# Kernel optimization log

Measured on AMD Instinct MI355X. Metric: run time of the kernel, lower is better.

The kernel has to match this reference:

```python
import jax, jax.numpy as jnp
import numpy as np

S, B, N, F, E, H, GH = 32, 64, 2048, 16, 32768, 512, 1
RNN_FEAT = N * GH
EPS = 1e-5


def setup_inputs() -> dict:
    key = jax.random.key(0)
    ks = jax.random.split(key, 24)
    f = lambda i, shape, s=0.1: (jax.random.normal(ks[i], shape, dtype=jnp.float32) * s)
    inp = {
        "x": jax.random.normal(ks[0], (S, B, N, F), dtype=jnp.float32),
        "edge_index": jax.random.randint(ks[1], (2, E), 0, N, dtype=jnp.int64),
        # GCNConv layers
        "W1": f(2, (F, GH)), "b1": f(3, (GH,)),
        "W2": f(4, (GH, GH)), "b2": f(5, (GH,)),
        # BatchNorm1d (eval mode: running stats)
        "gamma": jnp.ones((RNN_FEAT,), jnp.float32),
        "beta": jnp.zeros((RNN_FEAT,), jnp.float32),
        "rmean": f(6, (RNN_FEAT,), 0.01),
        "rvar": jnp.ones((RNN_FEAT,), jnp.float32),
        # GRU layer 0 (input RNN_FEAT -> hidden H)
        "Wih0": f(7, (3 * H, RNN_FEAT), 0.02), "Whh0": f(8, (3 * H, H), 0.02),
        "bih0": f(9, (3 * H,), 0.02), "bhh0": f(10, (3 * H,), 0.02),
        # GRU layer 1 (H -> H)
        "Wih1": f(11, (3 * H, H), 0.02), "Whh1": f(12, (3 * H, H), 0.02),
        "bih1": f(13, (3 * H,), 0.02), "bhh1": f(14, (3 * H,), 0.02),
        # final Linear(H -> 1)
        "Wlin": f(15, (1, H), 0.05), "blin": f(16, (1,), 0.05),
    }
    return inp


def _gru_layer(inp, Wih, Whh, bih, bhh):
    Hh = Whh.shape[1]

    def step(hprev, xt):
        gi = xt @ Wih.T + bih          # (B, 3H)
        gh = hprev @ Whh.T + bhh       # (B, 3H)
        ir, iz, inn = jnp.split(gi, 3, axis=-1)
        hr, hz, hn = jnp.split(gh, 3, axis=-1)
        r = jax.nn.sigmoid(ir + hr)
        z = jax.nn.sigmoid(iz + hz)
        n = jnp.tanh(inn + r * hn)
        hnew = (1.0 - z) * n + z * hprev
        return hnew, hnew

    h0 = jnp.zeros((inp.shape[1], Hh), dtype=inp.dtype)
    hT, ys = jax.lax.scan(step, h0, inp)
    return ys, hT


def reference(x, edge_index, W1, b1, W2, b2, gamma, beta, rmean, rvar,
              Wih0, Whh0, bih0, bhh0, Wih1, Whh1, bih1, bhh1, Wlin, blin):
    Sx, Bx, Nx, Fx = x.shape
    loop = jnp.arange(Nx, dtype=edge_index.dtype)
    src = jnp.concatenate([edge_index[0], loop])  # self-loops (GCNConv default)
    dst = jnp.concatenate([edge_index[1], loop])
    deg = jax.ops.segment_sum(jnp.ones_like(src, dtype=x.dtype), dst, num_segments=Nx)
    dinv = jax.lax.rsqrt(deg)  # deg >= 1 thanks to self-loops
    norm = dinv[src] * dinv[dst]  # (E+N,)

    def conv(h, W, b):
        h = h @ W                                           # (SB, N, F')
        m = (h[:, src, :] * norm[None, :, None])            # (SB, E+N, F')
        agg = jax.ops.segment_sum(m.transpose(1, 0, 2), dst, num_segments=Nx)
        return agg.transpose(1, 0, 2) + b                   # (SB, N, F')

    xr = x.reshape(Sx * Bx, Nx, Fx)
    h = jax.nn.sigmoid(conv(xr, W1, b1))   # dropout is identity in eval mode
    h = conv(h, W2, b2)                    # (SB, N, GH)
    o = h.reshape(Sx, Bx, Nx * h.shape[-1])
    # BatchNorm1d, eval mode
    o = (o - rmean) * jax.lax.rsqrt(rvar + EPS) * gamma + beta

    y1, h1 = _gru_layer(o, Wih0, Whh0, bih0, bhh0)
    y2, h2 = _gru_layer(y1, Wih1, Whh1, bih1, bhh1)
    out = y2 @ Wlin.T + blin               # (S, B, 1)
    hn = jnp.stack([h1, h2])               # (n_layers, B, H)
    return out, hn
```

## Files before the change

kernel.cpp:

```cpp
#include <hip/hip_runtime.h>
#include <stdint.h>

#define S_DIM 32
#define B_DIM 64
#define N_DIM 2048
#define F_DIM 16
#define E_DIM 32768
#define H_DIM 512
#define H3 1536
#define SB 2048
#define EPS_BN 1e-5f
#define GRUB 256

typedef __attribute__((ext_vector_type(4))) float f32x4;
typedef __attribute__((ext_vector_type(8))) __bf16 bf16x8;

static __device__ __forceinline__ unsigned short f2bf(float f) {
    union { float f; unsigned int u; } v; v.f = f;
    unsigned int r = v.u + 0x7FFFu + ((v.u >> 16) & 1u);
    return (unsigned short)(r >> 16);
}

#define HLD(dst, base, OFF) \
    asm volatile("global_load_dword %0, %1, off offset:" #OFF " sc0 sc1" : "=v"(dst) : "v"(base))
#define HLD16(A, I, base) \
    HLD(A[I+0],base,0);    HLD(A[I+1],base,256);  HLD(A[I+2],base,512);  HLD(A[I+3],base,768); \
    HLD(A[I+4],base,1024); HLD(A[I+5],base,1280); HLD(A[I+6],base,1536); HLD(A[I+7],base,1792); \
    HLD(A[I+8],base,2048); HLD(A[I+9],base,2304); HLD(A[I+10],base,2560);HLD(A[I+11],base,2816);\
    HLD(A[I+12],base,3072);HLD(A[I+13],base,3328);HLD(A[I+14],base,3584);HLD(A[I+15],base,3840)
#define HST(val, addr) \
    asm volatile("global_store_dword %0, %1, off sc0 sc1" :: "v"(addr), "v"(val) : "memory")

__global__ __launch_bounds__(256) void k_gcn1_dot(const float* __restrict__ x,
        const float* __restrict__ W1, float* __restrict__ z) {
    __shared__ float tile[64][65];
    int bn = blockIdx.x & 31;
    int bs = blockIdx.x >> 5;
    int n0 = bn * 64, sb0 = bs * 64;
    float4 w0 = *(const float4*)&W1[0];
    float4 w1 = *(const float4*)&W1[4];
    float4 w2 = *(const float4*)&W1[8];
    float4 w3 = *(const float4*)&W1[12];
    int t = threadIdx.x;
    for (int i = 0; i < 16; ++i) {
        int idx = t + 256 * i;
        int nl = idx & 63, sl = idx >> 6;
        const float4* xv = (const float4*)(x + ((size_t)(sb0 + sl) * N_DIM + (n0 + nl)) * F_DIM);
        float4 a = xv[0], b = xv[1], c = xv[2], d = xv[3];
        float acc = a.x*w0.x + a.y*w0.y + a.z*w0.z + a.w*w0.w
                  + b.x*w1.x + b.y*w1.y + b.z*w1.z + b.w*w1.w
                  + c.x*w2.x + c.y*w2.y + c.z*w2.z + c.w*w2.w
                  + d.x*w3.x + d.y*w3.y + d.z*w3.z + d.w*w3.w;
        tile[nl][sl] = acc;
    }
    __syncthreads();
    for (int i = 0; i < 16; ++i) {
        int idx = t + 256 * i;
        int sl = idx & 63, nl = idx >> 6;
        z[(size_t)(n0 + nl) * SB + sb0 + sl] = tile[nl][sl];
    }
}

__global__ void k_degcnt(const int* __restrict__ ei, int* __restrict__ cnt) {
    int e = blockIdx.x * 256 + threadIdx.x;
    if (e < E_DIM) atomicAdd(&cnt[ei[E_DIM + e]], 1);
}
__global__ void k_dinv(const int* __restrict__ cnt, float* __restrict__ dinv) {
    int n = blockIdx.x * 256 + threadIdx.x;
    if (n < N_DIM) dinv[n] = rsqrtf(1.0f + (float)cnt[n]);
}
__global__ void k_scan(const int* __restrict__ cnt, int* __restrict__ rowptr) {
    __shared__ int sc[2048];
    int t = threadIdx.x;
    sc[t] = cnt[t]; sc[t + 1024] = cnt[t + 1024];
    __syncthreads();
    for (int off = 1; off < 2048; off <<= 1) {
        int a = (t >= off) ? sc[t - off] : 0;
        int b = (t + 1024 >= off) ? sc[t + 1024 - off] : 0;
        __syncthreads();
        sc[t] += a; sc[t + 1024] += b;
        __syncthreads();
    }
    rowptr[t] = sc[t] - cnt[t];
    rowptr[t + 1024] = sc[t + 1024] - cnt[t + 1024];
    if (t == 0) rowptr[2048] = E_DIM;
}
__global__ void k_fill(const int* __restrict__ ei, const int* __restrict__ rowptr,
                       int* __restrict__ cursor, int* __restrict__ cols) {
    int e = blockIdx.x * 256 + threadIdx.x;
    if (e < E_DIM) {
        int d = ei[E_DIM + e];
        int pos = atomicAdd(&cursor[d], 1);
        cols[rowptr[d] + pos] = ei[e];
    }
}

__global__ __launch_bounds__(256) void k_spmm(const float* __restrict__ in,
        float* __restrict__ outp, const int* __restrict__ rowptr, const int* __restrict__ cols,
        const float* __restrict__ dinv, int mode,
        const float* __restrict__ bp, const float* __restrict__ w2p,
        const float* __restrict__ gamma, const float* __restrict__ beta,
        const float* __restrict__ rmean, const float* __restrict__ rvar) {
    int n = blockIdx.x & 2047;
    int sb = ((blockIdx.x >> 11) << 8) + threadIdx.x;
    float dn = dinv[n];
    float acc = dn * dn * in[(size_t)n * SB + sb];
    int i0 = rowptr[n], i1 = rowptr[n + 1];
    for (int idx = i0; idx < i1; ++idx) {
        int s = cols[idx];
        acc += dn * dinv[s] * in[(size_t)s * SB + sb];
    }
    float v;
    if (mode == 0) {
        v = acc + bp[0];
        v = 1.0f / (1.0f + __expf(-v));
    } else {
        v = w2p[0] * acc + bp[0];
        v = (v - rmean[n]) * rsqrtf(rvar[n] + EPS_BN) * gamma[n] + beta[n];
    }
    outp[(size_t)n * SB + sb] = v;
}

__global__ __launch_bounds__(256) void k_transpose_cvt(const float* __restrict__ in,
        unsigned short* __restrict__ outp, int R, int C) {
    __shared__ float tile[64][65];
    int nrt = R >> 6;
    int rt = blockIdx.x % nrt;
    int ct = blockIdx.x / nrt;
    int r0 = rt * 64, c0 = ct * 64;
    int t = threadIdx.x;
    for (int i = 0; i < 16; ++i) {
        int idx = t + i * 256;
        int cl = idx & 63, rl = idx >> 6;
        tile[rl][cl] = in[(size_t)(r0 + rl) * C + c0 + cl];
    }
    __syncthreads();
    for (int i = 0; i < 16; ++i) {
        int idx = t + i * 256;
        int rl = idx & 63, cl = idx >> 6;
        outp[(size_t)(c0 + cl) * R + r0 + rl] = f2bf(tile[rl][cl]);
    }
}

__global__ __launch_bounds__(256) void k_transpose_f32(const float* __restrict__ in,
        float* __restrict__ outp, int R, int C) {
    __shared__ float tile[64][65];
    int nrt = R >> 6;
    int rt = blockIdx.x % nrt;
    int ct = blockIdx.x / nrt;
    int r0 = rt * 64, c0 = ct * 64;
    int t = threadIdx.x;
    for (int i = 0; i < 16; ++i) {
        int idx = t + i * 256;
        int cl = idx & 63, rl = idx >> 6;
        tile[rl][cl] = in[(size_t)(r0 + rl) * C + c0 + cl];
    }
    __syncthreads();
    for (int i = 0; i < 16; ++i) {
        int idx = t + i * 256;
        int rl = idx & 63, cl = idx >> 6;
        outp[(size_t)(c0 + cl) * R + r0 + rl] = tile[rl][cl];
    }
}

__global__ void k_cvt_bf16(const float* __restrict__ in, unsigned short* __restrict__ outp, int nelem) {
    int i = (blockIdx.x * 256 + threadIdx.x) * 4;
    if (i < nelem) {
        float4 v = *(const float4*)&in[i];
        ushort4 o;
        o.x = f2bf(v.x); o.y = f2bf(v.y); o.z = f2bf(v.z); o.w = f2bf(v.w);
        *(ushort4*)&outp[i] = o;
    }
}

#define BM 128
#define BN 64
#define BKK 32
#define LDT 40

__global__ __launch_bounds__(256) void k_gemm_bf16(
        const unsigned short* __restrict__ A,
        const unsigned short* __restrict__ Bm,
        const float* __restrict__ bias,
        float* __restrict__ Cm, int M, int N, int K) {
    __shared__ __align__(16) unsigned short lA[BM * LDT];
    __shared__ __align__(16) unsigned short lB[BN * LDT];
    int mtiles = M / BM;
    int mt = blockIdx.x % mtiles;
    int nt = blockIdx.x / mtiles;
    int m0 = mt * BM, n0 = nt * BN;
    int t = threadIdx.x;
    int wave = t >> 6, lane = t & 63;
    int wm = (wave >> 1) * 64, wn = (wave & 1) * 32;
    int lrow = lane & 15, lk = (lane >> 4) * 8;
    int srowA = t >> 1, scolA = (t & 1) * 16;
    int srowB = t >> 2, scolB = (t & 3) * 8;
    f32x4 acc[4][2] = {};
    for (int k0 = 0; k0 < K; k0 += BKK) {
        const unsigned short* ga = A  + (size_t)(m0 + srowA) * K + k0 + scolA;
        const unsigned short* gb = Bm + (size_t)(n0 + srowB) * K + k0 + scolB;
        *(uint4*)&lA[srowA * LDT + scolA]     = *(const uint4*)ga;
        *(uint4*)&lA[srowA * LDT + scolA + 8] = *(const uint4*)(ga + 8);
        *(uint4*)&lB[srowB * LDT + scolB]     = *(const uint4*)gb;
        __syncthreads();
        bf16x8 af[4], bg[2];
        #pragma unroll
        for (int i = 0; i < 4; ++i)
            af[i] = *(const bf16x8*)&lA[(wm + i * 16 + lrow) * LDT + lk];
        #pragma unroll
        for (int j = 0; j < 2; ++j)
            bg[j] = *(const bf16x8*)&lB[(wn + j * 16 + lrow) * LDT + lk];
        #pragma unroll
        for (int i = 0; i < 4; ++i)
            #pragma unroll
            for (int j = 0; j < 2; ++j)
                acc[i][j] = __builtin_amdgcn_mfma_f32_16x16x32_bf16(af[i], bg[j], acc[i][j], 0, 0, 0);
        __syncthreads();
    }
    int crow = (lane >> 4) * 4, ccol = lane & 15;
    #pragma unroll
    for (int i = 0; i < 4; ++i)
        #pragma unroll
        for (int j = 0; j < 2; ++j) {
            int gn = n0 + wn + j * 16 + ccol;
            float bv = bias[gn];
            #pragma unroll
            for (int r = 0; r < 4; ++r) {
                int gm = m0 + wm + i * 16 + crow + r;
                Cm[(size_t)gm * N + gn] = acc[i][j][r] + bv;
            }
        }
}

__global__ __launch_bounds__(512, 2) void k_gru_layer(
        const float* __restrict__ giT,
        const float* __restrict__ Whh,
        const float* __restrict__ bhh,
        float* __restrict__ hTA,
        float* __restrict__ hTB,
        float* __restrict__ yT,
        float* __restrict__ hn_out,
        int* __restrict__ bar) {
    __shared__ float wlds[6 * 512];
    __shared__ float red[6][8][64];
    int tid = threadIdx.x;
    int lane = tid & 63;
    int wv = tid >> 6;
    int jh = blockIdx.x * 2 + (wv & 1);
    #pragma unroll
    for (int c = 0; c < 6; ++c)
        wlds[c * 512 + tid] = Whh[(size_t)((c % 3) * 512 + blockIdx.x * 2 + c / 3) * H_DIM + tid];
    __syncthreads();
    float br = bhh[jh], bz = bhh[512 + jh], bn = bhh[1024 + jh];
    const f32x4* wp0 = (const f32x4*)&wlds[0 * 512 + wv * 64];
    const f32x4* wp1 = (const f32x4*)&wlds[1 * 512 + wv * 64];
    const f32x4* wp2 = (const f32x4*)&wlds[2 * 512 + wv * 64];
    const f32x4* wp3 = (const f32x4*)&wlds[3 * 512 + wv * 64];
    const f32x4* wp4 = (const f32x4*)&wlds[4 * 512 + wv * 64];
    const f32x4* wp5 = (const f32x4*)&wlds[5 * 512 + wv * 64];
    float hp_reg = 0.0f;
    for (int t = 0; t < 32; ++t) {
        const float* hr = (t & 1) ? hTB : hTA;
        float* hw = (t & 1) ? hTA : hTB;
        float hreg[64];
        const float* hb0 = hr + (size_t)(wv * 64) * 64 + lane;
        const float* hb1 = hb0 + 1024;
        const float* hb2 = hb0 + 2048;
        const float* hb3 = hb0 + 3072;
        HLD16(hreg, 0, hb0); HLD16(hreg, 16, hb1);
        HLD16(hreg, 32, hb2); HLD16(hreg, 48, hb3);
        asm volatile("s_waitcnt vmcnt(0)" ::: "memory");
        __builtin_amdgcn_sched_barrier(0);
        float a0=0,a1=0,a2=0,a3=0,a4=0,a5=0;
        #pragma unroll
        for (int q = 0; q < 16; ++q) {
            float h0 = hreg[4*q], h1 = hreg[4*q+1], h2 = hreg[4*q+2], h3 = hreg[4*q+3];
            f32x4 v0 = wp0[q], v1 = wp1[q], v2 = wp2[q], v3 = wp3[q], v4 = wp4[q], v5 = wp5[q];
            a0 += h0*v0.x + h1*v0.y + h2*v0.z + h3*v0.w;
            a1 += h0*v1.x + h1*v1.y + h2*v1.z + h3*v1.w;
            a2 += h0*v2.x + h1*v2.y + h2*v2.z + h3*v2.w;
            a3 += h0*v3.x + h1*v3.y + h2*v3.z + h3*v3.w;
            a4 += h0*v4.x + h1*v4.y + h2*v4.z + h3*v4.w;
            a5 += h0*v5.x + h1*v5.y + h2*v5.z + h3*v5.w;
        }
        red[0][wv][lane] = a0; red[1][wv][lane] = a1; red[2][wv][lane] = a2;
        red[3][wv][lane] = a3; red[4][wv][lane] = a4; red[5][wv][lane] = a5;
        __syncthreads();
        if (wv < 2) {
            float ar = 0, az = 0, an = 0;
            #pragma unroll
            for (int q = 0; q < 8; ++q) {
                ar += red[wv * 3 + 0][q][lane];
                az += red[wv * 3 + 1][q][lane];
                an += red[wv * 3 + 2][q][lane];
            }
            int col = t * 64 + lane;
            float gr = giT[(size_t)jh * SB + col];
            float gz = giT[(size_t)(512 + jh) * SB + col];
            float gn = giT[(size_t)(1024 + jh) * SB + col];
            float rr = 1.0f / (1.0f + __expf(-(gr + ar + br)));
            float zz = 1.0f / (1.0f + __expf(-(gz + az + bz)));
            float nn = tanhf(gn + rr * (an + bn));
            float h = (1.0f - zz) * nn + zz * hp_reg;
            hp_reg = h;
            HST(h, hw + jh * 64 + lane);
            yT[(size_t)jh * SB + col] = h;
            if (t == 31) hn_out[lane * H_DIM + jh] = h;
            asm volatile("s_waitcnt vmcnt(0)" ::: "memory");
        }
        __syncthreads();
        if (tid == 0) {
            __hip_atomic_fetch_add(bar, 1, __ATOMIC_RELAXED, __HIP_MEMORY_SCOPE_AGENT);
            int tgt = (t + 1) * GRUB;
            while (__hip_atomic_load(bar, __ATOMIC_RELAXED, __HIP_MEMORY_SCOPE_AGENT) < tgt)
                __builtin_amdgcn_s_sleep(2);
        }
        __syncthreads();
    }
}

__global__ void k_final(const float* __restrict__ y2T, const float* __restrict__ Wlin,
                        const float* __restrict__ blin, float* __restrict__ outp) {
    int sb = blockIdx.x * 256 + threadIdx.x;
    float acc = blin[0];
    for (int k = 0; k < H_DIM; ++k)
        acc += y2T[(size_t)k * SB + sb] * Wlin[k];
    outp[sb] = acc;
}

extern "C" void kernel_launch(void* const* d_in, const int* in_sizes, int n_in,
                              void* d_out, int out_size, void* d_ws, size_t ws_size,
                              hipStream_t stream) {
    (void)in_sizes; (void)n_in; (void)out_size; (void)ws_size;
    const float* x     = (const float*)d_in[0];
    const int*   ei    = (const int*)d_in[1];
    const float* W1    = (const float*)d_in[2];
    const float* b1    = (const float*)d_in[3];
    const float* W2    = (const float*)d_in[4];
    const float* b2    = (const float*)d_in[5];
    const float* gamma = (const float*)d_in[6];
    const float* beta  = (const float*)d_in[7];
    const float* rmean = (const float*)d_in[8];
    const float* rvar  = (const float*)d_in[9];
    const float* Wih0  = (const float*)d_in[10];
    const float* Whh0  = (const float*)d_in[11];
    const float* bih0  = (const float*)d_in[12];
    const float* bhh0  = (const float*)d_in[13];
    const float* Wih1  = (const float*)d_in[14];
    const float* Whh1  = (const float*)d_in[15];
    const float* bih1  = (const float*)d_in[16];
    const float* bhh1  = (const float*)d_in[17];
    const float* Wlin  = (const float*)d_in[18];
    const float* blin  = (const float*)d_in[19];
    float* outp = (float*)d_out;

    char* w = (char*)d_ws;
    auto alloc = [&](size_t bytes) { char* p = w; w += (bytes + 255) & ~(size_t)255; return p; };
    float*          zbuf   = (float*)alloc((size_t)N_DIM * SB * 4);
    float*          h1buf  = (float*)alloc((size_t)N_DIM * SB * 4);
    float*          giT    = (float*)alloc((size_t)H3 * SB * 4);
    unsigned short* wih0b  = (unsigned short*)alloc((size_t)H3 * N_DIM * 2);
    unsigned short* wih1b  = (unsigned short*)alloc((size_t)H3 * H_DIM * 2);
    float*          y1T    = (float*)alloc((size_t)H_DIM * SB * 4);
    unsigned short* y1b    = (unsigned short*)alloc((size_t)SB * H_DIM * 2);
    float*          hTA    = (float*)alloc(H_DIM * B_DIM * 4);
    float*          hTB    = (float*)alloc(H_DIM * B_DIM * 4);
    float*          dinv   = (float*)alloc(N_DIM * 4);
    int*            degcnt = (int*)alloc(N_DIM * 4);
    int*            rowptr = (int*)alloc((N_DIM + 1) * 4);
    int*            cursor = (int*)alloc(N_DIM * 4);
    int*            cols   = (int*)alloc(E_DIM * 4);
    int*            bar0   = (int*)alloc(256);
    int*            bar1   = (int*)alloc(256);
    unsigned short* obf    = (unsigned short*)h1buf;

    hipMemsetAsync(degcnt, 0, N_DIM * 4, stream);
    hipMemsetAsync(cursor, 0, N_DIM * 4, stream);
    hipMemsetAsync(hTA, 0, H_DIM * B_DIM * 4, stream);
    hipMemsetAsync(bar0, 0, 256, stream);
    hipMemsetAsync(bar1, 0, 256, stream);

    k_gcn1_dot<<<1024, 256, 0, stream>>>(x, W1, zbuf);
    k_degcnt<<<E_DIM / 256, 256, 0, stream>>>(ei, degcnt);
    k_dinv<<<N_DIM / 256, 256, 0, stream>>>(degcnt, dinv);
    k_scan<<<1, 1024, 0, stream>>>(degcnt, rowptr);
    k_fill<<<E_DIM / 256, 256, 0, stream>>>(ei, rowptr, cursor, cols);

    k_spmm<<<16384, 256, 0, stream>>>(zbuf, h1buf, rowptr, cols, dinv, 0, b1, (const float*)nullptr,
                                      gamma, beta, rmean, rvar);
    k_spmm<<<16384, 256, 0, stream>>>(h1buf, zbuf, rowptr, cols, dinv, 1, b2, W2,
                                      gamma, beta, rmean, rvar);
    k_transpose_cvt<<<(N_DIM / 64) * (SB / 64), 256, 0, stream>>>(zbuf, obf, N_DIM, SB);
    k_cvt_bf16<<<(H3 * N_DIM / 4) / 256, 256, 0, stream>>>(Wih0, wih0b, H3 * N_DIM);
    k_cvt_bf16<<<(H3 * H_DIM / 4) / 256, 256, 0, stream>>>(Wih1, wih1b, H3 * H_DIM);

    float* gi0 = zbuf;
    k_gemm_bf16<<<(SB / BM) * (H3 / BN), 256, 0, stream>>>(obf, wih0b, bih0, gi0, SB, H3, N_DIM);
    k_transpose_f32<<<(SB / 64) * (H3 / 64), 256, 0, stream>>>(gi0, giT, SB, H3);

    k_gru_layer<<<GRUB, 512, 0, stream>>>(giT, Whh0, bhh0, hTA, hTB, y1T, outp + 2048, bar0);

    k_transpose_cvt<<<(H_DIM / 64) * (SB / 64), 256, 0, stream>>>(y1T, y1b, H_DIM, SB);
    float* gi1 = h1buf;
    k_gemm_bf16<<<(SB / BM) * (H3 / BN), 256, 0, stream>>>(y1b, wih1b, bih1, gi1, SB, H3, H_DIM);
    k_transpose_f32<<<(SB / 64) * (H3 / 64), 256, 0, stream>>>(gi1, giT, SB, H3);

    hipMemsetAsync(hTA, 0, H_DIM * B_DIM * 4, stream);
    k_gru_layer<<<GRUB, 512, 0, stream>>>(giT, Whh1, bhh1, hTA, hTB, y1T, outp + 2048 + 32768, bar1);

    k_final<<<SB / 256, 256, 0, stream>>>(y1T, Wlin, blin, outp);
}
```

Baseline: 1.181 ms.

## Fuse transposes into GEMM epilogue, hierarchical GRU barrier, prefetch gate inputs

Result: faster. 1.098 ms (-7.0%).

```diff
diff --git a/kernel.cpp b/kernel.cpp
--- a/kernel.cpp
+++ b/kernel.cpp
@@ -65,14 +65,12 @@
     int e = blockIdx.x * 256 + threadIdx.x;
     if (e < E_DIM) atomicAdd(&cnt[ei[E_DIM + e]], 1);
 }
-__global__ void k_dinv(const int* __restrict__ cnt, float* __restrict__ dinv) {
-    int n = blockIdx.x * 256 + threadIdx.x;
-    if (n < N_DIM) dinv[n] = rsqrtf(1.0f + (float)cnt[n]);
-}
-__global__ void k_scan(const int* __restrict__ cnt, int* __restrict__ rowptr) {
+__global__ void k_scan(const int* __restrict__ cnt, int* __restrict__ rowptr,
+                       float* __restrict__ dinv) {
     __shared__ int sc[2048];
     int t = threadIdx.x;
-    sc[t] = cnt[t]; sc[t + 1024] = cnt[t + 1024];
+    int c0 = cnt[t], c1 = cnt[t + 1024];
+    sc[t] = c0; sc[t + 1024] = c1;
     __syncthreads();
     for (int off = 1; off < 2048; off <<= 1) {
         int a = (t >= off) ? sc[t - off] : 0;
@@ -81,9 +79,11 @@
         sc[t] += a; sc[t + 1024] += b;
         __syncthreads();
     }
-    rowptr[t] = sc[t] - cnt[t];
-    rowptr[t + 1024] = sc[t + 1024] - cnt[t + 1024];
+    rowptr[t] = sc[t] - c0;
+    rowptr[t + 1024] = sc[t + 1024] - c1;
     if (t == 0) rowptr[2048] = E_DIM;
+    dinv[t] = rsqrtf(1.0f + (float)c0);
+    dinv[t + 1024] = rsqrtf(1.0f + (float)c1);
 }
 __global__ void k_fill(const int* __restrict__ ei, const int* __restrict__ rowptr,
                        int* __restrict__ cursor, int* __restrict__ cols) {
@@ -142,27 +142,6 @@
     }
 }
 
-__global__ __launch_bounds__(256) void k_transpose_f32(const float* __restrict__ in,
-        float* __restrict__ outp, int R, int C) {
-    __shared__ float tile[64][65];
-    int nrt = R >> 6;
-    int rt = blockIdx.x % nrt;
-    int ct = blockIdx.x / nrt;
-    int r0 = rt * 64, c0 = ct * 64;
-    int t = threadIdx.x;
-    for (int i = 0; i < 16; ++i) {
-        int idx = t + i * 256;
-        int cl = idx & 63, rl = idx >> 6;
-        tile[rl][cl] = in[(size_t)(r0 + rl) * C + c0 + cl];
-    }
-    __syncthreads();
-    for (int i = 0; i < 16; ++i) {
-        int idx = t + i * 256;
-        int rl = idx & 63, cl = idx >> 6;
-        outp[(size_t)(c0 + cl) * R + r0 + rl] = tile[rl][cl];
-    }
-}
-
 __global__ void k_cvt_bf16(const float* __restrict__ in, unsigned short* __restrict__ outp, int nelem) {
     int i = (blockIdx.x * 256 + threadIdx.x) * 4;
     if (i < nelem) {
@@ -178,11 +157,11 @@
 #define BKK 32
 #define LDT 40
 
-__global__ __launch_bounds__(256) void k_gemm_bf16(
+__global__ __launch_bounds__(256) void k_gemm_bf16_t(
         const unsigned short* __restrict__ A,
         const unsigned short* __restrict__ Bm,
         const float* __restrict__ bias,
-        float* __restrict__ Cm, int M, int N, int K) {
+        float* __restrict__ CT, int M, int N, int K) {
     __shared__ __align__(16) unsigned short lA[BM * LDT];
     __shared__ __align__(16) unsigned short lB[BN * LDT];
     int mtiles = M / BM;
@@ -223,12 +202,12 @@
         #pragma unroll
         for (int j = 0; j < 2; ++j) {
             int gn = n0 + wn + j * 16 + ccol;
+            int gm = m0 + wm + i * 16 + crow;
             float bv = bias[gn];
-            #pragma unroll
-            for (int r = 0; r < 4; ++r) {
-                int gm = m0 + wm + i * 16 + crow + r;
-                Cm[(size_t)gm * N + gn] = acc[i][j][r] + bv;
-            }
+            float4 v;
+            v.x = acc[i][j][0] + bv; v.y = acc[i][j][1] + bv;
+            v.z = acc[i][j][2] + bv; v.w = acc[i][j][3] + bv;
+            *(float4*)&CT[(size_t)gn * M + gm] = v;
         }
 }
 
@@ -258,10 +237,18 @@
     const f32x4* wp3 = (const f32x4*)&wlds[3 * 512 + wv * 64];
     const f32x4* wp4 = (const f32x4*)&wlds[4 * 512 + wv * 64];
     const f32x4* wp5 = (const f32x4*)&wlds[5 * 512 + wv * 64];
+    int* leaf = bar + 32 + ((blockIdx.x >> 5) << 5);
     float hp_reg = 0.0f;
     for (int t = 0; t < 32; ++t) {
         const float* hr = (t & 1) ? hTB : hTA;
         float* hw = (t & 1) ? hTA : hTB;
+        float gr_p = 0.f, gz_p = 0.f, gn_p = 0.f;
+        int col = t * 64 + lane;
+        if (wv < 2) {
+            gr_p = giT[(size_t)jh * SB + col];
+            gz_p = giT[(size_t)(512 + jh) * SB + col];
+            gn_p = giT[(size_t)(1024 + jh) * SB + col];
+        }
         float hreg[64];
         const float* hb0 = hr + (size_t)(wv * 64) * 64 + lane;
         const float* hb1 = hb0 + 1024;
@@ -286,6 +273,7 @@
         red[0][wv][lane] = a0; red[1][wv][lane] = a1; red[2][wv][lane] = a2;
         red[3][wv][lane] = a3; red[4][wv][lane] = a4; red[5][wv][lane] = a5;
         __syncthreads();
+        float h_new = 0.f;
         if (wv < 2) {
             float ar = 0, az = 0, an = 0;
             #pragma unroll
@@ -294,25 +282,29 @@
                 az += red[wv * 3 + 1][q][lane];
                 an += red[wv * 3 + 2][q][lane];
             }
-            int col = t * 64 + lane;
-            float gr = giT[(size_t)jh * SB + col];
-            float gz = giT[(size_t)(512 + jh) * SB + col];
-            float gn = giT[(size_t)(1024 + jh) * SB + col];
-            float rr = 1.0f / (1.0f + __expf(-(gr + ar + br)));
-            float zz = 1.0f / (1.0f + __expf(-(gz + az + bz)));
-            float nn = tanhf(gn + rr * (an + bn));
-            float h = (1.0f - zz) * nn + zz * hp_reg;
-            hp_reg = h;
-            HST(h, hw + jh * 64 + lane);
-            yT[(size_t)jh * SB + col] = h;
-            if (t == 31) hn_out[lane * H_DIM + jh] = h;
+            float rr = 1.0f / (1.0f + __expf(-(gr_p + ar + br)));
+            float zz = 1.0f / (1.0f + __expf(-(gz_p + az + bz)));
+            float nn = tanhf(gn_p + rr * (an + bn));
+            h_new = (1.0f - zz) * nn + zz * hp_reg;
+            hp_reg = h_new;
+            HST(h_new, hw + jh * 64 + lane);
             asm volatile("s_waitcnt vmcnt(0)" ::: "memory");
         }
         __syncthreads();
         if (tid == 0) {
-            __hip_atomic_fetch_add(bar, 1, __ATOMIC_RELAXED, __HIP_MEMORY_SCOPE_AGENT);
-            int tgt = (t + 1) * GRUB;
-            while (__hip_atomic_load(bar, __ATOMIC_RELAXED, __HIP_MEMORY_SCOPE_AGENT) < tgt)
+            int old = __hip_atomic_fetch_add(leaf, 1, __ATOMIC_RELAXED, __HIP_MEMORY_SCOPE_AGENT);
+            if ((old & 31) == 31) {
+                int r = __hip_atomic_fetch_add(bar + 16, 1, __ATOMIC_RELAXED, __HIP_MEMORY_SCOPE_AGENT);
+                if ((r & 7) == 7)
+                    __hip_atomic_store(bar, t + 1, __ATOMIC_RELAXED, __HIP_MEMORY_SCOPE_AGENT);
+            }
+        }
+        if (wv < 2) {
+            yT[(size_t)jh * SB + col] = h_new;
+            if (t == 31) hn_out[lane * H_DIM + jh] = h_new;
+        }
+        if (tid == 0) {
+            while (__hip_atomic_load(bar, __ATOMIC_RELAXED, __HIP_MEMORY_SCOPE_AGENT) < t + 1)
                 __builtin_amdgcn_s_sleep(2);
         }
         __syncthreads();
@@ -370,20 +362,19 @@
     int*            rowptr = (int*)alloc((N_DIM + 1) * 4);
     int*            cursor = (int*)alloc(N_DIM * 4);
     int*            cols   = (int*)alloc(E_DIM * 4);
-    int*            bar0   = (int*)alloc(256);
-    int*            bar1   = (int*)alloc(256);
+    int*            bar0   = (int*)alloc(2048);
+    int*            bar1   = (int*)alloc(2048);
     unsigned short* obf    = (unsigned short*)h1buf;
 
     hipMemsetAsync(degcnt, 0, N_DIM * 4, stream);
     hipMemsetAsync(cursor, 0, N_DIM * 4, stream);
     hipMemsetAsync(hTA, 0, H_DIM * B_DIM * 4, stream);
-    hipMemsetAsync(bar0, 0, 256, stream);
-    hipMemsetAsync(bar1, 0, 256, stream);
+    hipMemsetAsync(bar0, 0, 2048, stream);
+    hipMemsetAsync(bar1, 0, 2048, stream);
 
     k_gcn1_dot<<<1024, 256, 0, stream>>>(x, W1, zbuf);
     k_degcnt<<<E_DIM / 256, 256, 0, stream>>>(ei, degcnt);
-    k_dinv<<<N_DIM / 256, 256, 0, stream>>>(degcnt, dinv);
-    k_scan<<<1, 1024, 0, stream>>>(degcnt, rowptr);
+    k_scan<<<1, 1024, 0, stream>>>(degcnt, rowptr, dinv);
     k_fill<<<E_DIM / 256, 256, 0, stream>>>(ei, rowptr, cursor, cols);
 
     k_spmm<<<16384, 256, 0, stream>>>(zbuf, h1buf, rowptr, cols, dinv, 0, b1, (const float*)nullptr,
@@ -394,16 +385,12 @@
     k_cvt_bf16<<<(H3 * N_DIM / 4) / 256, 256, 0, stream>>>(Wih0, wih0b, H3 * N_DIM);
     k_cvt_bf16<<<(H3 * H_DIM / 4) / 256, 256, 0, stream>>>(Wih1, wih1b, H3 * H_DIM);
 
-    float* gi0 = zbuf;
-    k_gemm_bf16<<<(SB / BM) * (H3 / BN), 256, 0, stream>>>(obf, wih0b, bih0, gi0, SB, H3, N_DIM);
-    k_transpose_f32<<<(SB / 64) * (H3 / 64), 256, 0, stream>>>(gi0, giT, SB, H3);
+    k_gemm_bf16_t<<<(SB / BM) * (H3 / BN), 256, 0, stream>>>(obf, wih0b, bih0, giT, SB, H3, N_DIM);
 
     k_gru_layer<<<GRUB, 512, 0, stream>>>(giT, Whh0, bhh0, hTA, hTB, y1T, outp + 2048, bar0);
 
     k_transpose_cvt<<<(H_DIM / 64) * (SB / 64), 256, 0, stream>>>(y1T, y1b, H_DIM, SB);
-    float* gi1 = h1buf;
-    k_gemm_bf16<<<(SB / BM) * (H3 / BN), 256, 0, stream>>>(y1b, wih1b, bih1, gi1, SB, H3, H_DIM);
-    k_transpose_f32<<<(SB / 64) * (H3 / 64), 256, 0, stream>>>(gi1, giT, SB, H3);
+    k_gemm_bf16_t<<<(SB / BM) * (H3 / BN), 256, 0, stream>>>(y1b, wih1b, bih1, giT, SB, H3, H_DIM);
 
     hipMemsetAsync(hTA, 0, H_DIM * B_DIM * 4, stream);
     k_gru_layer<<<GRUB, 512, 0, stream>>>(giT, Whh1, bhh1, hTA, hTB, y1T, outp + 2048 + 32768, bar1);
```
